# Performance work log

Measured on AMD Instinct MI355X. Metric: run time of the kernel, lower is better.

The kernel has to match this reference:

```python
import jax, jax.numpy as jnp
import numpy as np

B, T, D, V, LMAX = 16, 512, 256, 4233, 64
NEG = -1e30  # finite 'log zero' keeps grads NaN-free


def setup_inputs() -> dict:
    key = jax.random.key(0)
    k1, k2, k3, k4 = jax.random.split(key, 4)
    hs_pad = jax.random.normal(k1, (B, T, D), dtype=jnp.float32)
    hlens = jnp.full((B,), T, dtype=jnp.int32)
    ys_pad = jax.random.randint(k2, (B, LMAX), 1, V, dtype=jnp.int32)  # blank=0 excluded
    ys_lens = jax.random.randint(k3, (B,), LMAX // 2, LMAX + 1, dtype=jnp.int32)
    W = jax.random.normal(k4, (V, D), dtype=jnp.float32) * (1.0 / np.sqrt(D))
    b = jnp.zeros((V,), dtype=jnp.float32)
    return {"hs_pad": hs_pad, "hlens": hlens, "ys_pad": ys_pad,
            "ys_lens": ys_lens, "W": W, "b": b}


def _ctc_loss_sum(logp_tbv, ext, allow, hlens, ys_lens):
    """logp_tbv: [T,B,V] log-softmax; ext: [B,S] extended labels (blank-interleaved).
    Returns sum over batch of -log p(y|x) (torch CTCLoss reduction='sum')."""
    Tn, Bn, _ = logp_tbv.shape
    S = ext.shape[1]
    # per-frame log-prob of each extended label: [T,B,S]
    lp_ext = jnp.take_along_axis(
        logp_tbv, jnp.broadcast_to(ext[None], (Tn, Bn, S)), axis=2)

    # t = 0 init: alpha[0]=lp(blank), alpha[1]=lp(y_1)
    alpha0 = jnp.full((Bn, S), NEG, dtype=logp_tbv.dtype)
    alpha0 = alpha0.at[:, 0].set(lp_ext[0, :, 0])
    alpha0 = alpha0.at[:, 1].set(lp_ext[0, :, 1])

    def step(alpha, inp):
        lp_t, t = inp  # lp_t: [B,S]
        a1 = jnp.pad(alpha[:, :-1], ((0, 0), (1, 0)), constant_values=NEG)
        a2 = jnp.pad(alpha[:, :-2], ((0, 0), (2, 0)), constant_values=NEG)
        a2 = jnp.where(allow, a2, NEG)
        new = jnp.logaddexp(jnp.logaddexp(alpha, a1), a2) + lp_t
        alpha = jnp.where((t < hlens)[:, None], new, alpha)  # freeze past hlen
        return alpha, None

    ts = jnp.arange(1, Tn, dtype=jnp.int32)
    alpha, _ = jax.lax.scan(step, alpha0, (lp_ext[1:], ts))

    last = 2 * ys_lens  # index of final blank state
    bi = jnp.arange(Bn)
    ll = jnp.logaddexp(alpha[bi, last], alpha[bi, last - 1])
    return -jnp.sum(ll)


def reference(hs_pad, hlens, ys_pad, ys_lens, W, b):
    # linear projection + log_softmax (dropout_rate=0.0 -> identity)
    logits = jnp.einsum('btd,vd->btv', hs_pad, W) + b
    logp = jax.nn.log_softmax(logits, axis=-1)          # [B,T,V]
    logp = jnp.transpose(logp, (1, 0, 2))               # [T,B,V]

    Bn, Lmax = ys_pad.shape
    S = 2 * Lmax + 1
    ext = jnp.zeros((Bn, S), dtype=ys_pad.dtype).at[:, 1::2].set(ys_pad)
    prev2 = jnp.pad(ext, ((0, 0), (2, 0)))[:, :-2]
    allow = (ext != 0) & (ext != prev2) & (jnp.arange(S) >= 2)

    loss = _ctc_loss_sum(logp, ext, allow, hlens, ys_lens)
    return loss / Bn  # module divides by ys_hat.size(1) == batch
```

## Files before the change

kernel.cpp:

```cpp
#include <hip/hip_runtime.h>

constexpr int Bn = 16;
constexpr int Tn = 512;
constexpr int Dn = 256;
constexpr int Vn = 4233;
constexpr int Vp = 4352;
constexpr int Ln = 64;
constexpr int Un = 80;
constexpr int CS = 68;
constexpr int NCB = 34;
constexpr int Mtot = Bn * Tn;

#define LN2     0.6931471805599453f
#define INV_LN2 1.4426950408889634f

typedef __attribute__((ext_vector_type(8))) short short8;
typedef __attribute__((ext_vector_type(4))) float f32x4;

__device__ __forceinline__ float lg2(float x) { return __builtin_amdgcn_logf(x); }
__device__ __forceinline__ float ex2(float x) { return __builtin_amdgcn_exp2f(x); }

__device__ __forceinline__ unsigned short cvt_bf16(float f) {
    unsigned int u = __float_as_uint(f);
    u = (u + 0x7fffu + ((u >> 16) & 1u)) >> 16;
    return (unsigned short)u;
}

__device__ __forceinline__ void gl_lds16(const void* g, void* l) {
    __builtin_amdgcn_global_load_lds(
        (const __attribute__((address_space(1))) void*)g,
        (__attribute__((address_space(3))) void*)l,
        16, 0, 0);
}

__device__ __forceinline__ float dpp_shr1_f(float v, float edge) {
    return __int_as_float(__builtin_amdgcn_update_dpp(
        __float_as_int(edge), __float_as_int(v), 0x138, 0xF, 0xF, false));
}
__device__ __forceinline__ int dpp_shr1_i(int v, int edge) {
    return __builtin_amdgcn_update_dpp(edge, v, 0x138, 0xF, 0xF, false);
}

__global__ __launch_bounds__(256) void conv(
    const float* __restrict__ hs, const float* __restrict__ W,
    const float* __restrict__ bias, const int* __restrict__ ys,
    unsigned short* __restrict__ hs_b, unsigned short* __restrict__ w_b,
    float* __restrict__ gbias, float* __restrict__ out)
{
    const int gid = blockIdx.x * 256 + threadIdx.x;
    const int stride = gridDim.x * 256;
    const float4* hs4 = (const float4*)hs;
    const float4* W4  = (const float4*)W;

    if (gid == 0) out[0] = 0.0f;

    for (int i = gid; i < (Bn * Tn * Dn) / 4; i += stride) {
        float4 v = hs4[i];
        ushort4 o = make_ushort4(cvt_bf16(v.x), cvt_bf16(v.y), cvt_bf16(v.z), cvt_bf16(v.w));
        *(ushort4*)(&hs_b[i * 4]) = o;
    }
    for (int i = gid; i < Vp * (Dn / 4); i += stride) {
        int row = i >> 6;
        float4 v = make_float4(0.f, 0.f, 0.f, 0.f);
        if (row < Vn) v = W4[i];
        ushort4 o = make_ushort4(cvt_bf16(v.x), cvt_bf16(v.y), cvt_bf16(v.z), cvt_bf16(v.w));
        *(ushort4*)(&w_b[i * 4]) = o;
    }
    for (int i = gid; i < Bn * 128; i += stride) {
        int b = i >> 7;
        int u = i & 127;
        int v = (u == 0) ? 0 : ((u <= Ln) ? ys[b * Ln + u - 1] : -1);
        gbias[i] = (v >= 0) ? bias[v] : 0.0f;
    }
}

__global__ __launch_bounds__(256) void gemm_se(
    const unsigned short* __restrict__ hs_b, const unsigned short* __restrict__ w_b,
    const int* __restrict__ ys, const float* __restrict__ bias,
    const float* __restrict__ gbias, float* __restrict__ sep,
    float* __restrict__ glg2)
{
    __shared__ __align__(16) short lsA[128 * 64];
    __shared__ __align__(16) short lsB[128 * 64];

    const int tid = threadIdx.x;
    const int lane = tid & 63;
    const int w = tid >> 6;
    const int lr = lane & 15;
    const int kq = lane >> 4;
    const int m0 = blockIdx.x * 128;
    const int mw = w * 32;
    const bool gather = (blockIdx.y == NCB);
    const int b = blockIdx.x >> 2;

    const int srow = lane >> 3;
    const int scg  = (lane & 7) ^ (srow & 7);
    const int scol = scg * 8;

    const unsigned short* bptr[4];
    #pragma unroll
    for (int j = 0; j < 4; ++j) {
        int c = w * 4 + j;
        int row = c * 8 + srow;
        int v;
        if (gather) {
            if (row == 0) v = 0;
            else if (row <= Ln) v = ys[b * Ln + row - 1];
            else v = Vn + 32;
        } else {
            v = blockIdx.y * 128 + row;
        }
        bptr[j] = w_b + (size_t)v * Dn + scol;
    }

    f32x4 acc[2][8];
    #pragma unroll
    for (int mf = 0; mf < 2; ++mf)
        #pragma unroll
        for (int nf = 0; nf < 8; ++nf)
            acc[mf][nf] = (f32x4){0.f, 0.f, 0.f, 0.f};

    for (int ks = 0; ks < 4; ++ks) {
        const int k0 = ks * 64;
        __syncthreads();
        #pragma unroll
        for (int j = 0; j < 4; ++j) {
            int c = w * 4 + j;
            int row = c * 8 + srow;
            gl_lds16(hs_b + (size_t)(m0 + row) * Dn + k0 + scol, (char*)lsA + c * 1024);
            gl_lds16(bptr[j] + k0,                               (char*)lsB + c * 1024);
        }
        __syncthreads();

        #pragma unroll
        for (int sub = 0; sub < 2; ++sub) {
            short8 af[2], bf[8];
            #pragma unroll
            for (int mf = 0; mf < 2; ++mf) {
                int row = mw + mf * 16 + lr;
                int cg = (sub * 4 + kq) ^ (row & 7);
                af[mf] = *(const short8*)(&lsA[row * 64 + cg * 8]);
            }
            #pragma unroll
            for (int nf = 0; nf < 8; ++nf) {
                int row = nf * 16 + lr;
                int cg = (sub * 4 + kq) ^ (row & 7);
                bf[nf] = *(const short8*)(&lsB[row * 64 + cg * 8]);
            }
            #pragma unroll
            for (int mf = 0; mf < 2; ++mf)
                #pragma unroll
                for (int nf = 0; nf < 8; ++nf)
                    acc[mf][nf] = __builtin_amdgcn_mfma_f32_16x16x32_bf16(
                        af[mf], bf[nf], acc[mf][nf], 0, 0, 0);
        }
    }

    if (!gather) {
        const int n0 = blockIdx.y * 128;
        float bcol[8]; bool valid[8];
        #pragma unroll
        for (int nf = 0; nf < 8; ++nf) {
            int col = n0 + nf * 16 + lr;
            valid[nf] = (col < Vn);
            bcol[nf] = valid[nf] ? bias[col] : 0.0f;
        }
        #pragma unroll
        for (int mf = 0; mf < 2; ++mf) {
            #pragma unroll
            for (int r = 0; r < 4; ++r) {
                float s = 0.0f;
                #pragma unroll
                for (int nf = 0; nf < 8; ++nf)
                    if (valid[nf]) s += __expf(acc[mf][nf][r] + bcol[nf]);
                #pragma unroll
                for (int off = 1; off < 16; off <<= 1) s += __shfl_xor(s, off, 64);
                if (lr == 0)
                    sep[(size_t)blockIdx.y * Mtot + m0 + mw + mf * 16 + kq * 4 + r] = s;
            }
        }
    } else {
        #pragma unroll
        for (int mf = 0; mf < 2; ++mf) {
            #pragma unroll
            for (int nf = 0; nf < 5; ++nf) {
                int u = nf * 16 + lr;
                float gv = gbias[b * 128 + u];
                #pragma unroll
                for (int r = 0; r < 4; ++r) {
                    int g = m0 + mw + mf * 16 + kq * 4 + r;
                    glg2[(size_t)g * Un + u] = (acc[mf][nf][r] + gv) * INV_LN2;
                }
            }
        }
    }
}

__global__ __launch_bounds__(256) void lse_norm(
    const float* __restrict__ sep, float* __restrict__ glg2)
{
    __shared__ float sl[64];
    const int tid = threadIdx.x;
    const int g0 = blockIdx.x * 64;

    if (tid < 64) {
        float s = 0.0f;
        #pragma unroll
        for (int c = 0; c < NCB; ++c) s += sep[(size_t)c * Mtot + g0 + tid];
        sl[tid] = lg2(s);
    }
    __syncthreads();

    #pragma unroll
    for (int j = 0; j < 4; ++j) {
        int i = tid + j * 256;
        int row = i >> 4, u4 = (i & 15) * 4;
        float* p = glg2 + (size_t)(g0 + row) * Un + u4;
        float4 v = *(const float4*)p;
        float sub = sl[row];
        v.x = ex2(v.x - sub); v.y = ex2(v.y - sub);
        v.z = ex2(v.z - sub); v.w = ex2(v.w - sub);
        *(float4*)p = v;
    }
    if (tid < 64) {
        float* p = glg2 + (size_t)(g0 + tid) * Un + 64;
        *p = ex2(*p - sl[tid]);
    }
}

__global__ __launch_bounds__(256) void ctc_fwd(
    const float* __restrict__ pmat, const int* __restrict__ ys,
    const int* __restrict__ hlens, const int* __restrict__ ylens,
    float* __restrict__ out)
{
    __shared__ float ls[2][64 * CS + 4];
    __shared__ float shO[64], shE[64], shZ[64];
    __shared__ int   shX[64];

    const int b = blockIdx.x;
    const int tid = threadIdx.x;
    const int l = tid & 63;

    const int hl = hlens[b];
    int yl  = ys[b * Ln + l];
    int ylm = (l >= 1) ? ys[b * Ln + l - 1] : -1;
    const float aF = ((l >= 1) && (yl != ylm)) ? 1.0f : 0.0f;

    const float* pm = pmat + (size_t)b * Tn * Un;

    #pragma unroll
    for (int j = 0; j < 4; ++j) {
        int i = tid + j * 256;
        int tt = i >> 4, u4 = (i & 15) * 4;
        *(float4*)(&ls[0][tt * CS + u4]) = *(const float4*)(pm + (size_t)(1 + tt) * Un + u4);
    }
    if (tid < 64) ls[0][tid * CS + 64] = pm[(size_t)(1 + tid) * Un + 64];
    __syncthreads();

    float o = (l == 0) ? pm[1] : 0.0f;
    float e = (l == 0) ? pm[0] : 0.0f;
    float z = 0.0f;
    int ex = 0;
    int dn = 0;

    float4 r4a = make_float4(0.f,0.f,0.f,0.f), r4b = r4a, r4c = r4a, r4d = r4a;
    float r1 = 0.0f;

    float qa0, qa1, qa2, qa3, ra0, ra1, ra2, ra3;
    float qb0, qb1, qb2, qb3, rb0, rb1, rb2, rb3;
    float qc0, qc1, qc2, qc3, rc0, rc1, rc2, rc3;

#define RENORM do { \
        float mm = fmaxf(fmaxf(o, e), z); \
        bool nz = (mm > 0.0f); \
        int dd = nz ? ((int)((__float_as_uint(mm) >> 23) & 255u) - 127) : 0; \
        o = ldexpf(o, -dd); e = ldexpf(e, -dd); z = ldexpf(z, -dd); \
        int exT = ex + dd; \
        int xm1 = dpp_shr1_i(exT, -(1 << 28)); \
        int et = nz ? exT : xm1; \
        ex = et; \
        int xet = dpp_shr1_i(et, -(1 << 28)); \
        dn = xet - ex; \
    } while (0)

#define STEPR(qv, rv) do { \
        float om1 = dpp_shr1_f(o, 0.0f); \
        float an  = ldexpf(om1, dn); \
        float nO = fmaf(aF, an, o + e) * (rv); \
        float nE = (e + an) * (qv); \
        float nZ = (z + o) * (qv); \
        o = nO; e = nE; z = nZ; \
    } while (0)

#define LDA(base) do { \
        qa0 = buf[(base) * CS];       ra0 = buf[(base) * CS + 1 + l]; \
        qa1 = buf[((base)+1) * CS];   ra1 = buf[((base)+1) * CS + 1 + l]; \
        qa2 = buf[((base)+2) * CS];   ra2 = buf[((base)+2) * CS + 1 + l]; \
        qa3 = buf[((base)+3) * CS];   ra3 = buf[((base)+3) * CS + 1 + l]; \
    } while (0)
#define LDB(base) do { \
        qb0 = buf[(base) * CS];       rb0 = buf[(base) * CS + 1 + l]; \
        qb1 = buf[((base)+1) * CS];   rb1 = buf[((base)+1) * CS + 1 + l]; \
        qb2 = buf[((base)+2) * CS];   rb2 = buf[((base)+2) * CS + 1 + l]; \
        qb3 = buf[((base)+3) * CS];   rb3 = buf[((base)+3) * CS + 1 + l]; \
    } while (0)
#define LDC(base) do { \
        qc0 = buf[(base) * CS];       rc0 = buf[(base) * CS + 1 + l]; \
        qc1 = buf[((base)+1) * CS];   rc1 = buf[((base)+1) * CS + 1 + l]; \
        qc2 = buf[((base)+2) * CS];   rc2 = buf[((base)+2) * CS + 1 + l]; \
        qc3 = buf[((base)+3) * CS];   rc3 = buf[((base)+3) * CS + 1 + l]; \
    } while (0)

#define W4A do { RENORM; STEPR(qa0,ra0); STEPR(qa1,ra1); STEPR(qa2,ra2); STEPR(qa3,ra3); } while (0)
#define W4B do { RENORM; STEPR(qb0,rb0); STEPR(qb1,rb1); STEPR(qb2,rb2); STEPR(qb3,rb3); } while (0)
#define W4C do { RENORM; STEPR(qc0,rc0); STEPR(qc1,rc1); STEPR(qc2,rc2); STEPR(qc3,rc3); } while (0)

#define STEPS(Joff, ACT) do { \
        RENORM; \
        float q = buf[(Joff) * CS]; \
        float r = buf[(Joff) * CS + 1 + l]; \
        float om1 = dpp_shr1_f(o, 0.0f); \
        float an  = ldexpf(om1, dn); \
        float nO = fmaf(aF, an, o + e) * r; \
        float nE = (e + an) * q; \
        float nZ = (z + o) * q; \
        bool act = (ACT); \
        o = act ? nO : o; e = act ? nE : e; z = act ? nZ : z; \
    } while (0)

    for (int c = 0; c < 8; ++c) {
        if (c < 7) {
            const int tb = 1 + (c + 1) * 64;
            { int i = tid;       int tt = i >> 4, u4 = (i & 15) * 4;
              r4a = (tb + tt < Tn) ? *(const float4*)(pm + (size_t)(tb + tt) * Un + u4) : make_float4(0.f,0.f,0.f,0.f); }
            { int i = tid + 256; int tt = i >> 4, u4 = (i & 15) * 4;
              r4b = (tb + tt < Tn) ? *(const float4*)(pm + (size_t)(tb + tt) * Un + u4) : make_float4(0.f,0.f,0.f,0.f); }
            { int i = tid + 512; int tt = i >> 4, u4 = (i & 15) * 4;
              r4c = (tb + tt < Tn) ? *(const float4*)(pm + (size_t)(tb + tt) * Un + u4) : make_float4(0.f,0.f,0.f,0.f); }
            { int i = tid + 768; int tt = i >> 4, u4 = (i & 15) * 4;
              r4d = (tb + tt < Tn) ? *(const float4*)(pm + (size_t)(tb + tt) * Un + u4) : make_float4(0.f,0.f,0.f,0.f); }
            if (tid < 64)
                r1 = (tb + tid < Tn) ? pm[(size_t)(tb + tid) * Un + 64] : 0.0f;
        }

        const float* buf = ls[c & 1];

        if (c < 7) {
            if (hl >= (c + 1) * 64 + 1) {
                LDA(0); LDB(4);
                LDC(8);  W4A;
                LDA(12); W4B;
                LDB(16); W4C;
                LDC(20); W4A;
                LDA(24); W4B;
                LDB(28); W4C;
                LDC(32); W4A;
                LDA(36); W4B;
                LDB(40); W4C;
                LDC(44); W4A;
                LDA(48); W4B;
                LDB(52); W4C;
                LDC(56); W4A;
                LDA(60); W4B;
                W4C;
                W4A;
            } else {
                #pragma unroll 1
                for (int j = 0; j < 64; ++j)
                    STEPS(j, (c * 64 + 1 + j) < hl);
            }
        } else {
            if (hl >= Tn) {
                LDA(0); LDB(4);
                LDC(8);  W4A;
                LDA(12); W4B;
                LDB(16); W4C;
                LDC(20); W4A;
                LDA(24); W4B;
                LDB(28); W4C;
                LDC(32); W4A;
                LDA(36); W4B;
                LDB(40); W4C;
                LDC(44); W4A;
                LDA(48); W4B;
                LDB(52); W4C;
                LDC(56); W4A;
                LDA(60); W4B;
                W4C;
                RENORM;
                STEPR(qa0, ra0); STEPR(qa1, ra1); STEPR(qa2, ra2);
            } else {
                #pragma unroll 1
                for (int j = 0; j < 63; ++j)
                    STEPS(j, (449 + j) < hl);
            }
        }

        if (c < 7) {
            float* dst = ls[(c + 1) & 1];
            { int i = tid;       int tt = i >> 4, u4 = (i & 15) * 4; *(float4*)(&dst[tt * CS + u4]) = r4a; }
            { int i = tid + 256; int tt = i >> 4, u4 = (i & 15) * 4; *(float4*)(&dst[tt * CS + u4]) = r4b; }
            { int i = tid + 512; int tt = i >> 4, u4 = (i & 15) * 4; *(float4*)(&dst[tt * CS + u4]) = r4c; }
            { int i = tid + 768; int tt = i >> 4, u4 = (i & 15) * 4; *(float4*)(&dst[tt * CS + u4]) = r4d; }
            if (tid < 64) dst[tid * CS + 64] = r1;
        }
        __syncthreads();
    }
#undef RENORM
#undef STEPR
#undef LDA
#undef LDB
#undef LDC
#undef W4A
#undef W4B
#undef W4C
#undef STEPS

    if (tid < 64) { shO[l] = o; shE[l] = e; shZ[l] = z; shX[l] = ex; }
    __syncthreads();

    if (tid == 0) {
        int L = ylens[b];
        float vo = shO[L - 1]; int xo = shX[L - 1];
        float ve; int xe;
        if (L == 64) { ve = shZ[63]; xe = shX[63]; }
        else         { ve = shE[L];  xe = shX[L]; }
        int em = (xo > xe) ? xo : xe;
        float s = ldexpf(vo, xo - em) + ldexpf(ve, xe - em);
        float ll = (lg2(s) + (float)em) * LN2;
        atomicAdd(out, -ll / (float)Bn);
    }
}

extern "C" void kernel_launch(void* const* d_in, const int* in_sizes, int n_in,
                              void* d_out, int out_size, void* d_ws, size_t ws_size,
                              hipStream_t stream) {
    const float* hs    = (const float*)d_in[0];
    const int*   hlens = (const int*)d_in[1];
    const int*   ys    = (const int*)d_in[2];
    const int*   ylens = (const int*)d_in[3];
    const float* W     = (const float*)d_in[4];
    const float* bias  = (const float*)d_in[5];
    float* out = (float*)d_out;

    char* ws = (char*)d_ws;
    unsigned short* hs_b = (unsigned short*)(ws);
    unsigned short* w_b  = (unsigned short*)(ws + 4194304);
    float* glg2  = (float*)(ws + 6422528);
    float* sep   = (float*)(ws + 9043968);
    float* gbias = (float*)(ws + 10158080);

    conv<<<1024, 256, 0, stream>>>(hs, W, bias, ys, hs_b, w_b, gbias, out);
    gemm_se<<<dim3(64, NCB + 1), 256, 0, stream>>>(hs_b, w_b, ys, bias, gbias, sep, glg2);
    lse_norm<<<Mtot / 64, 256, 0, stream>>>(sep, glg2);
    ctc_fwd<<<Bn, 256, 0, stream>>>(glg2, ys, hlens, ylens, out);
}
```

Before: 123.8 us.

## Fuse GEMM, normalization and CTC forward into one persistent kernel with counters

Merges the GEMM/sum-exp, log-sum-exp normalization and CTC forward kernels into a single launch. The first 16 blocks run the CTC recursion and spin-wait on per-row-tile atomic counters, so each 128-row chunk can be consumed as soon as its GEMM blocks finish. The normalization pass is dropped: raw log2 gathered values are exponentiated on load, and the per-frame log-normalizer is summed by a helper wave and subtracted from the final log-likelihood. This removes two launches and a full read/write pass over the gathered probabilities. It relies on the CTC blocks being scheduled alongside the GEMM blocks without deadlock, and one wave now fetches while another accumulates corrections.

```diff
diff --git a/kernel.cpp b/kernel.cpp
--- a/kernel.cpp
+++ b/kernel.cpp
@@ -45,7 +45,7 @@
     const float* __restrict__ hs, const float* __restrict__ W,
     const float* __restrict__ bias, const int* __restrict__ ys,
     unsigned short* __restrict__ hs_b, unsigned short* __restrict__ w_b,
-    float* __restrict__ gbias, float* __restrict__ out)
+    float* __restrict__ gbias, float* __restrict__ out, int* __restrict__ cnt)
 {
     const int gid = blockIdx.x * 256 + threadIdx.x;
     const int stride = gridDim.x * 256;
@@ -53,6 +53,7 @@
     const float4* W4  = (const float4*)W;
 
     if (gid == 0) out[0] = 0.0f;
+    if (gid < 64) cnt[gid] = 0;
 
     for (int i = gid; i < (Bn * Tn * Dn) / 4; i += stride) {
         float4 v = hs4[i];
@@ -74,197 +75,183 @@
     }
 }
 
-__global__ __launch_bounds__(256) void gemm_se(
+__global__ __launch_bounds__(256) void mega(
     const unsigned short* __restrict__ hs_b, const unsigned short* __restrict__ w_b,
     const int* __restrict__ ys, const float* __restrict__ bias,
     const float* __restrict__ gbias, float* __restrict__ sep,
-    float* __restrict__ glg2)
+    float* __restrict__ glg2, const int* __restrict__ hlens,
+    const int* __restrict__ ylens, float* __restrict__ out,
+    int* __restrict__ cnt)
 {
-    __shared__ __align__(16) short lsA[128 * 64];
-    __shared__ __align__(16) short lsB[128 * 64];
+    __shared__ __align__(16) union SMem {
+        struct { short A[128 * 64]; short Bt[128 * 64]; } g;
+        struct {
+            float ls[2][64 * CS + 4];
+            float shO[64], shE[64], shZ[64];
+            int   shX[64];
+            float corr0, corrS;
+        } c;
+    } sm;
 
     const int tid = threadIdx.x;
     const int lane = tid & 63;
     const int w = tid >> 6;
-    const int lr = lane & 15;
-    const int kq = lane >> 4;
-    const int m0 = blockIdx.x * 128;
-    const int mw = w * 32;
-    const bool gather = (blockIdx.y == NCB);
-    const int b = blockIdx.x >> 2;
-
-    const int srow = lane >> 3;
-    const int scg  = (lane & 7) ^ (srow & 7);
-    const int scol = scg * 8;
-
-    const unsigned short* bptr[4];
-    #pragma unroll
-    for (int j = 0; j < 4; ++j) {
-        int c = w * 4 + j;
-        int row = c * 8 + srow;
-        int v;
-        if (gather) {
-            if (row == 0) v = 0;
-            else if (row <= Ln) v = ys[b * Ln + row - 1];
-            else v = Vn + 32;
-        } else {
-            v = blockIdx.y * 128 + row;
-        }
-        bptr[j] = w_b + (size_t)v * Dn + scol;
-    }
-
-    f32x4 acc[2][8];
-    #pragma unroll
-    for (int mf = 0; mf < 2; ++mf)
-        #pragma unroll
-        for (int nf = 0; nf < 8; ++nf)
-            acc[mf][nf] = (f32x4){0.f, 0.f, 0.f, 0.f};
-
-    for (int ks = 0; ks < 4; ++ks) {
-        const int k0 = ks * 64;
-        __syncthreads();
+
+    if (blockIdx.x >= 16) {
+        const int gidb = blockIdx.x - 16;
+        const int bx = gidb / 35;
+        const int by = gidb - bx * 35;
+        const bool gather = (by == NCB);
+        const int m0 = bx * 128;
+        const int mw = w * 32;
+        const int b = bx >> 2;
+        const int lr = lane & 15;
+        const int kq = lane >> 4;
+
+        const int srow = lane >> 3;
+        const int scg  = (lane & 7) ^ (srow & 7);
+        const int scol = scg * 8;
+
+        const unsigned short* bptr[4];
         #pragma unroll
         for (int j = 0; j < 4; ++j) {
             int c = w * 4 + j;
             int row = c * 8 + srow;
-            gl_lds16(hs_b + (size_t)(m0 + row) * Dn + k0 + scol, (char*)lsA + c * 1024);
-            gl_lds16(bptr[j] + k0,                               (char*)lsB + c * 1024);
+            int v;
+            if (gather) {
+                if (row == 0) v = 0;
+                else if (row <= Ln) v = ys[b * Ln + row - 1];
+                else v = Vn + 32;
+            } else {
+                v = by * 128 + row;
+            }
+            bptr[j] = w_b + (size_t)v * Dn + scol;
         }
+
+        f32x4 acc[2][8];
+        #pragma unroll
+        for (int mf = 0; mf < 2; ++mf)
+            #pragma unroll
+            for (int nf = 0; nf < 8; ++nf)
+                acc[mf][nf] = (f32x4){0.f, 0.f, 0.f, 0.f};
+
+        for (int ks = 0; ks < 4; ++ks) {
+            const int k0 = ks * 64;
+            __syncthreads();
+            #pragma unroll
+            for (int j = 0; j < 4; ++j) {
+                int c = w * 4 + j;
+                int row = c * 8 + srow;
+                gl_lds16(hs_b + (size_t)(m0 + row) * Dn + k0 + scol, (char*)sm.g.A  + c * 1024);
+                gl_lds16(bptr[j] + k0,                               (char*)sm.g.Bt + c * 1024);
+            }
+            __syncthreads();
+
+            #pragma unroll
+            for (int sub = 0; sub < 2; ++sub) {
+                short8 af[2], bf[8];
+                #pragma unroll
+                for (int mf = 0; mf < 2; ++mf) {
+                    int row = mw + mf * 16 + lr;
+                    int cg = (sub * 4 + kq) ^ (row & 7);
+                    af[mf] = *(const short8*)(&sm.g.A[row * 64 + cg * 8]);
+                }
+                #pragma unroll
+                for (int nf = 0; nf < 8; ++nf) {
+                    int row = nf * 16 + lr;
+                    int cg = (sub * 4 + kq) ^ (row & 7);
+                    bf[nf] = *(const short8*)(&sm.g.Bt[row * 64 + cg * 8]);
+                }
+                #pragma unroll
+                for (int mf = 0; mf < 2; ++mf)
+                    #pragma unroll
+                    for (int nf = 0; nf < 8; ++nf)
+                        acc[mf][nf] = __builtin_amdgcn_mfma_f32_16x16x32_bf16(
+                            af[mf], bf[nf], acc[mf][nf], 0, 0, 0);
+            }
+        }
+
+        if (!gather) {
+            const int n0 = by * 128;
+            float bcol[8]; bool valid[8];
+            #pragma unroll
+            for (int nf = 0; nf < 8; ++nf) {
+                int col = n0 + nf * 16 + lr;
+                valid[nf] = (col < Vn);
+                bcol[nf] = valid[nf] ? bias[col] : 0.0f;
+            }
+            #pragma unroll
+            for (int mf = 0; mf < 2; ++mf) {
+                #pragma unroll
+                for (int r = 0; r < 4; ++r) {
+                    float s = 0.0f;
+                    #pragma unroll
+                    for (int nf = 0; nf < 8; ++nf)
+                        if (valid[nf]) s += __expf(acc[mf][nf][r] + bcol[nf]);
+                    #pragma unroll
+                    for (int off = 1; off < 16; off <<= 1) s += __shfl_xor(s, off, 64);
+                    if (lr == 0)
+                        sep[(size_t)by * Mtot + m0 + mw + mf * 16 + kq * 4 + r] = s;
+                }
+            }
+        } else {
+            #pragma unroll
+            for (int mf = 0; mf < 2; ++mf) {
+                #pragma unroll
+                for (int nf = 0; nf < 5; ++nf) {
+                    int u = nf * 16 + lr;
+                    float gv = gbias[b * 128 + u];
+                    #pragma unroll
+                    for (int r = 0; r < 4; ++r) {
+                        int gm = m0 + mw + mf * 16 + kq * 4 + r;
+                        glg2[(size_t)gm * Un + u] = (acc[mf][nf][r] + gv) * INV_LN2;
+                    }
+                }
+            }
+        }
+
         __syncthreads();
-
-        #pragma unroll
-        for (int sub = 0; sub < 2; ++sub) {
-            short8 af[2], bf[8];
-            #pragma unroll
-            for (int mf = 0; mf < 2; ++mf) {
-                int row = mw + mf * 16 + lr;
-                int cg = (sub * 4 + kq) ^ (row & 7);
-                af[mf] = *(const short8*)(&lsA[row * 64 + cg * 8]);
-            }
-            #pragma unroll
-            for (int nf = 0; nf < 8; ++nf) {
-                int row = nf * 16 + lr;
-                int cg = (sub * 4 + kq) ^ (row & 7);
-                bf[nf] = *(const short8*)(&lsB[row * 64 + cg * 8]);
-            }
-            #pragma unroll
-            for (int mf = 0; mf < 2; ++mf)
-                #pragma unroll
-                for (int nf = 0; nf < 8; ++nf)
-                    acc[mf][nf] = __builtin_amdgcn_mfma_f32_16x16x32_bf16(
-                        af[mf], bf[nf], acc[mf][nf], 0, 0, 0);
-        }
-    }
-
-    if (!gather) {
-        const int n0 = blockIdx.y * 128;
-        float bcol[8]; bool valid[8];
-        #pragma unroll
-        for (int nf = 0; nf < 8; ++nf) {
-            int col = n0 + nf * 16 + lr;
-            valid[nf] = (col < Vn);
-            bcol[nf] = valid[nf] ? bias[col] : 0.0f;
-        }
-        #pragma unroll
-        for (int mf = 0; mf < 2; ++mf) {
-            #pragma unroll
-            for (int r = 0; r < 4; ++r) {
-                float s = 0.0f;
-                #pragma unroll
-                for (int nf = 0; nf < 8; ++nf)
-                    if (valid[nf]) s += __expf(acc[mf][nf][r] + bcol[nf]);
-                #pragma unroll
-                for (int off = 1; off < 16; off <<= 1) s += __shfl_xor(s, off, 64);
-                if (lr == 0)
-                    sep[(size_t)blockIdx.y * Mtot + m0 + mw + mf * 16 + kq * 4 + r] = s;
-            }
-        }
-    } else {
-        #pragma unroll
-        for (int mf = 0; mf < 2; ++mf) {
-            #pragma unroll
-            for (int nf = 0; nf < 5; ++nf) {
-                int u = nf * 16 + lr;
-                float gv = gbias[b * 128 + u];
-                #pragma unroll
-                for (int r = 0; r < 4; ++r) {
-                    int g = m0 + mw + mf * 16 + kq * 4 + r;
-                    glg2[(size_t)g * Un + u] = (acc[mf][nf][r] + gv) * INV_LN2;
-                }
-            }
-        }
-    }
-}
-
-__global__ __launch_bounds__(256) void lse_norm(
-    const float* __restrict__ sep, float* __restrict__ glg2)
-{
-    __shared__ float sl[64];
-    const int tid = threadIdx.x;
-    const int g0 = blockIdx.x * 64;
-
-    if (tid < 64) {
-        float s = 0.0f;
-        #pragma unroll
-        for (int c = 0; c < NCB; ++c) s += sep[(size_t)c * Mtot + g0 + tid];
-        sl[tid] = lg2(s);
-    }
-    __syncthreads();
-
-    #pragma unroll
-    for (int j = 0; j < 4; ++j) {
-        int i = tid + j * 256;
-        int row = i >> 4, u4 = (i & 15) * 4;
-        float* p = glg2 + (size_t)(g0 + row) * Un + u4;
-        float4 v = *(const float4*)p;
-        float sub = sl[row];
-        v.x = ex2(v.x - sub); v.y = ex2(v.y - sub);
-        v.z = ex2(v.z - sub); v.w = ex2(v.w - sub);
-        *(float4*)p = v;
-    }
-    if (tid < 64) {
-        float* p = glg2 + (size_t)(g0 + tid) * Un + 64;
-        *p = ex2(*p - sl[tid]);
-    }
-}
-
-__global__ __launch_bounds__(256) void ctc_fwd(
-    const float* __restrict__ pmat, const int* __restrict__ ys,
-    const int* __restrict__ hlens, const int* __restrict__ ylens,
-    float* __restrict__ out)
-{
-    __shared__ float ls[2][64 * CS + 4];
-    __shared__ float shO[64], shE[64], shZ[64];
-    __shared__ int   shX[64];
+        if (tid == 0)
+            __hip_atomic_fetch_add(&cnt[bx], 1, __ATOMIC_RELEASE, __HIP_MEMORY_SCOPE_AGENT);
+        return;
+    }
 
     const int b = blockIdx.x;
-    const int tid = threadIdx.x;
-    const int l = tid & 63;
+    const int l = lane;
 
     const int hl = hlens[b];
     int yl  = ys[b * Ln + l];
     int ylm = (l >= 1) ? ys[b * Ln + l - 1] : -1;
     const float aF = ((l >= 1) && (yl != ylm)) ? 1.0f : 0.0f;
 
-    const float* pm = pmat + (size_t)b * Tn * Un;
+    const float* pm = glg2 + (size_t)b * Tn * Un;
+
+    while (__hip_atomic_load(&cnt[b * 4], __ATOMIC_ACQUIRE, __HIP_MEMORY_SCOPE_AGENT) < 35)
+        __builtin_amdgcn_s_sleep(8);
 
     #pragma unroll
     for (int j = 0; j < 4; ++j) {
         int i = tid + j * 256;
         int tt = i >> 4, u4 = (i & 15) * 4;
-        *(float4*)(&ls[0][tt * CS + u4]) = *(const float4*)(pm + (size_t)(1 + tt) * Un + u4);
-    }
-    if (tid < 64) ls[0][tid * CS + 64] = pm[(size_t)(1 + tid) * Un + 64];
+        float4 v = *(const float4*)(pm + (size_t)(1 + tt) * Un + u4);
+        v.x = ex2(v.x); v.y = ex2(v.y); v.z = ex2(v.z); v.w = ex2(v.w);
+        *(float4*)(&sm.c.ls[0][tt * CS + u4]) = v;
+    }
+    if (tid < 64) sm.c.ls[0][tid * CS + 64] = ex2(pm[(size_t)(1 + tid) * Un + 64]);
+    if (tid == 128) {
+        float s0 = 0.0f;
+        #pragma unroll
+        for (int cb = 0; cb < NCB; ++cb) s0 += sep[(size_t)cb * Mtot + b * Tn];
+        sm.c.corr0 = lg2(s0);
+    }
     __syncthreads();
 
-    float o = (l == 0) ? pm[1] : 0.0f;
-    float e = (l == 0) ? pm[0] : 0.0f;
+    float o = (l == 0) ? ex2(pm[1]) : 0.0f;
+    float e = (l == 0) ? ex2(pm[0]) : 0.0f;
     float z = 0.0f;
     int ex = 0;
     int dn = 0;
-
-    float4 r4a = make_float4(0.f,0.f,0.f,0.f), r4b = r4a, r4c = r4a, r4d = r4a;
-    float r1 = 0.0f;
+    float corr = 0.0f;
 
     float qa0, qa1, qa2, qa3, ra0, ra1, ra2, ra3;
     float qb0, qb1, qb2, qb3, rb0, rb1, rb2, rb3;
@@ -329,80 +316,97 @@
     } while (0)
 
     for (int c = 0; c < 8; ++c) {
-        if (c < 7) {
-            const int tb = 1 + (c + 1) * 64;
-            { int i = tid;       int tt = i >> 4, u4 = (i & 15) * 4;
-              r4a = (tb + tt < Tn) ? *(const float4*)(pm + (size_t)(tb + tt) * Un + u4) : make_float4(0.f,0.f,0.f,0.f); }
-            { int i = tid + 256; int tt = i >> 4, u4 = (i & 15) * 4;
-              r4b = (tb + tt < Tn) ? *(const float4*)(pm + (size_t)(tb + tt) * Un + u4) : make_float4(0.f,0.f,0.f,0.f); }
-            { int i = tid + 512; int tt = i >> 4, u4 = (i & 15) * 4;
-              r4c = (tb + tt < Tn) ? *(const float4*)(pm + (size_t)(tb + tt) * Un + u4) : make_float4(0.f,0.f,0.f,0.f); }
-            { int i = tid + 768; int tt = i >> 4, u4 = (i & 15) * 4;
-              r4d = (tb + tt < Tn) ? *(const float4*)(pm + (size_t)(tb + tt) * Un + u4) : make_float4(0.f,0.f,0.f,0.f); }
-            if (tid < 64)
-                r1 = (tb + tid < Tn) ? pm[(size_t)(tb + tid) * Un + 64] : 0.0f;
-        }
-
-        const float* buf = ls[c & 1];
-
-        if (c < 7) {
-            if (hl >= (c + 1) * 64 + 1) {
-                LDA(0); LDB(4);
-                LDC(8);  W4A;
-                LDA(12); W4B;
-                LDB(16); W4C;
-                LDC(20); W4A;
-                LDA(24); W4B;
-                LDB(28); W4C;
-                LDC(32); W4A;
-                LDA(36); W4B;
-                LDB(40); W4C;
-                LDC(44); W4A;
-                LDA(48); W4B;
-                LDB(52); W4C;
-                LDC(56); W4A;
-                LDA(60); W4B;
-                W4C;
-                W4A;
+        if (w == 0) {
+            const float* buf = sm.c.ls[c & 1];
+            if (c < 7) {
+                if (hl >= (c + 1) * 64 + 1) {
+                    LDA(0); LDB(4);
+                    LDC(8);  W4A;
+                    LDA(12); W4B;
+                    LDB(16); W4C;
+                    LDC(20); W4A;
+                    LDA(24); W4B;
+                    LDB(28); W4C;
+                    LDC(32); W4A;
+                    LDA(36); W4B;
+                    LDB(40); W4C;
+                    LDC(44); W4A;
+                    LDA(48); W4B;
+                    LDB(52); W4C;
+                    LDC(56); W4A;
+                    LDA(60); W4B;
+                    W4C;
+                    W4A;
+                } else {
+                    #pragma unroll 1
+                    for (int j = 0; j < 64; ++j)
+                        STEPS(j, (c * 64 + 1 + j) < hl);
+                }
             } else {
-                #pragma unroll 1
-                for (int j = 0; j < 64; ++j)
-                    STEPS(j, (c * 64 + 1 + j) < hl);
+                if (hl >= Tn) {
+                    LDA(0); LDB(4);
+                    LDC(8);  W4A;
+                    LDA(12); W4B;
+                    LDB(16); W4C;
+                    LDC(20); W4A;
+                    LDA(24); W4B;
+                    LDB(28); W4C;
+                    LDC(32); W4A;
+                    LDA(36); W4B;
+                    LDB(40); W4C;
+                    LDC(44); W4A;
+                    LDA(48); W4B;
+                    LDB(52); W4C;
+                    LDC(56); W4A;
+                    LDA(60); W4B;
+                    W4C;
+                    RENORM;
+                    STEPR(qa0, ra0); STEPR(qa1, ra1); STEPR(qa2, ra2);
+                } else {
+                    #pragma unroll 1
+                    for (int j = 0; j < 63; ++j)
+                        STEPS(j, (449 + j) < hl);
+                }
             }
         } else {
-            if (hl >= Tn) {
-                LDA(0); LDB(4);
-                LDC(8);  W4A;
-                LDA(12); W4B;
-                LDB(16); W4C;
-                LDC(20); W4A;
-                LDA(24); W4B;
-                LDB(28); W4C;
-                LDC(32); W4A;
-                LDA(36); W4B;
-                LDB(40); W4C;
-                LDC(44); W4A;
-                LDA(48); W4B;
-                LDB(52); W4C;
-                LDC(56); W4A;
-                LDA(60); W4B;
-                W4C;
-                RENORM;
-                STEPR(qa0, ra0); STEPR(qa1, ra1); STEPR(qa2, ra2);
-            } else {
-                #pragma unroll 1
-                for (int j = 0; j < 63; ++j)
-                    STEPS(j, (449 + j) < hl);
-            }
-        }
-
-        if (c < 7) {
-            float* dst = ls[(c + 1) & 1];
-            { int i = tid;       int tt = i >> 4, u4 = (i & 15) * 4; *(float4*)(&dst[tt * CS + u4]) = r4a; }
-            { int i = tid + 256; int tt = i >> 4, u4 = (i & 15) * 4; *(float4*)(&dst[tt * CS + u4]) = r4b; }
-            { int i = tid + 512; int tt = i >> 4, u4 = (i & 15) * 4; *(float4*)(&dst[tt * CS + u4]) = r4c; }
-            { int i = tid + 768; int tt = i >> 4, u4 = (i & 15) * 4; *(float4*)(&dst[tt * CS + u4]) = r4d; }
-            if (tid < 64) dst[tid * CS + 64] = r1;
+            if (c < 7) {
+                int p = (c + 2) >> 1; if (p > 3) p = 3;
+                while (__hip_atomic_load(&cnt[b * 4 + p], __ATOMIC_ACQUIRE, __HIP_MEMORY_SCOPE_AGENT) < 35)
+                    __builtin_amdgcn_s_sleep(8);
+
+                const int tb = 1 + (c + 1) * 64;
+                float* dst = sm.c.ls[(c + 1) & 1];
+                const int t192 = tid - 64;
+                #pragma unroll
+                for (int j = 0; j < 6; ++j) {
+                    int i = t192 + j * 192;
+                    if (i < 1024) {
+                        int tt = i >> 4, u4 = (i & 15) * 4;
+                        float4 v;
+                        if (tb + tt < Tn) {
+                            v = *(const float4*)(pm + (size_t)(tb + tt) * Un + u4);
+                            v.x = ex2(v.x); v.y = ex2(v.y); v.z = ex2(v.z); v.w = ex2(v.w);
+                        } else {
+                            v = make_float4(0.f, 0.f, 0.f, 0.f);
+                        }
+                        *(float4*)(&dst[tt * CS + u4]) = v;
+                    }
+                }
+                if (t192 >= 128) {
+                    int tt = t192 - 128;
+                    dst[tt * CS + 64] = (tb + tt < Tn) ? ex2(pm[(size_t)(tb + tt) * Un + 64]) : 0.0f;
+                }
+            }
+            if (w == 1) {
+                int t = c * 64 + 1 + l;
+                if (t < hl) {
+                    float s = 0.0f;
+                    #pragma unroll
+                    for (int cb = 0; cb < NCB; ++cb)
+                        s += sep[(size_t)cb * Mtot + b * Tn + t];
+                    corr += lg2(s);
+                }
+            }
         }
         __syncthreads();
     }
@@ -416,18 +420,24 @@
 #undef W4C
 #undef STEPS
 
-    if (tid < 64) { shO[l] = o; shE[l] = e; shZ[l] = z; shX[l] = ex; }
+    if (tid < 64) { sm.c.shO[l] = o; sm.c.shE[l] = e; sm.c.shZ[l] = z; sm.c.shX[l] = ex; }
+    if (w == 1) {
+        #pragma unroll
+        for (int off = 1; off < 64; off <<= 1) corr += __shfl_xor(corr, off, 64);
+        if (l == 0) sm.c.corrS = corr;
+    }
     __syncthreads();
 
     if (tid == 0) {
         int L = ylens[b];
-        float vo = shO[L - 1]; int xo = shX[L - 1];
+        float vo = sm.c.shO[L - 1]; int xo = sm.c.shX[L - 1];
         float ve; int xe;
-        if (L == 64) { ve = shZ[63]; xe = shX[63]; }
-        else         { ve = shE[L];  xe = shX[L]; }
+        if (L == 64) { ve = sm.c.shZ[63]; xe = sm.c.shX[63]; }
+        else         { ve = sm.c.shE[L];  xe = sm.c.shX[L]; }
         int em = (xo > xe) ? xo : xe;
         float s = ldexpf(vo, xo - em) + ldexpf(ve, xe - em);
-        float ll = (lg2(s) + (float)em) * LN2;
+        float corrT = sm.c.corrS + sm.c.corr0;
+        float ll = (lg2(s) + (float)em - corrT) * LN2;
         atomicAdd(out, -ll / (float)Bn);
     }
 }
@@ -449,9 +459,9 @@
     float* glg2  = (float*)(ws + 6422528);
     float* sep   = (float*)(ws + 9043968);
     float* gbias = (float*)(ws + 10158080);
-
-    conv<<<1024, 256, 0, stream>>>(hs, W, bias, ys, hs_b, w_b, gbias, out);
-    gemm_se<<<dim3(64, NCB + 1), 256, 0, stream>>>(hs_b, w_b, ys, bias, gbias, sep, glg2);
-    lse_norm<<<Mtot / 64, 256, 0, stream>>>(sep, glg2);
-    ctc_fwd<<<Bn, 256, 0, stream>>>(glg2, ys, hlens, ylens, out);
-}
+    int*   cnt   = (int*)(ws + 10166272);
+
+    conv<<<1024, 256, 0, stream>>>(hs, W, bias, ys, hs_b, w_b, gbias, out, cnt);
+    mega<<<16 + 64 * (NCB + 1), 256, 0, stream>>>(
+        hs_b, w_b, ys, bias, gbias, sep, glg2, hlens, ylens, out, cnt);
+}
```

After: 167.3 us. +35.1%, slower.

## Run CTC alpha recursion in fp64 with wave-uniform renormalization every 32 steps

Applied to the files above, without the earlier changes.

Switches the CTC forward recursion state from fp32 with per-lane exponents, renormalised every 4 steps, to fp64 with one wave-wide exponent. Renormalisation now runs only every 32 steps and uses a DPP/readlane max reduction. The wider dynamic range of double lets the code drop the per-step ldexp shift between neighbouring lanes and most of the renorm overhead. The cost is fp64 arithmetic, two DPP moves per shift and higher register pressure, and fp64 throughput on the target may or may not offset the removed work.

```diff
diff --git a/kernel.cpp b/kernel.cpp
--- a/kernel.cpp
+++ b/kernel.cpp
@@ -33,12 +33,27 @@
         16, 0, 0);
 }
 
-__device__ __forceinline__ float dpp_shr1_f(float v, float edge) {
-    return __int_as_float(__builtin_amdgcn_update_dpp(
-        __float_as_int(edge), __float_as_int(v), 0x138, 0xF, 0xF, false));
-}
-__device__ __forceinline__ int dpp_shr1_i(int v, int edge) {
-    return __builtin_amdgcn_update_dpp(edge, v, 0x138, 0xF, 0xF, false);
+__device__ __forceinline__ double dpp_shr1_d(double v) {
+    union { double d; int i[2]; } u, r;
+    u.d = v;
+    r.i[0] = __builtin_amdgcn_update_dpp(0, u.i[0], 0x138, 0xF, 0xF, false);
+    r.i[1] = __builtin_amdgcn_update_dpp(0, u.i[1], 0x138, 0xF, 0xF, false);
+    return r.d;
+}
+
+__device__ __forceinline__ int wave_imax(int v) {
+    int t;
+    t = __builtin_amdgcn_update_dpp(v, v, 0xB1,  0xF, 0xF, false); v = (t > v) ? t : v;
+    t = __builtin_amdgcn_update_dpp(v, v, 0x4E,  0xF, 0xF, false); v = (t > v) ? t : v;
+    t = __builtin_amdgcn_update_dpp(v, v, 0x141, 0xF, 0xF, false); v = (t > v) ? t : v;
+    t = __builtin_amdgcn_update_dpp(v, v, 0x140, 0xF, 0xF, false); v = (t > v) ? t : v;
+    int a = __builtin_amdgcn_readlane(v, 0);
+    int b = __builtin_amdgcn_readlane(v, 16);
+    int c = __builtin_amdgcn_readlane(v, 32);
+    int d = __builtin_amdgcn_readlane(v, 48);
+    int ab = (a > b) ? a : b;
+    int cd = (c > d) ? c : d;
+    return (ab > cd) ? ab : cd;
 }
 
 __global__ __launch_bounds__(256) void conv(
@@ -234,7 +249,7 @@
     float* __restrict__ out)
 {
     __shared__ float ls[2][64 * CS + 4];
-    __shared__ float shO[64], shE[64], shZ[64];
+    __shared__ double shO[64], shE[64], shZ[64];
     __shared__ int   shX[64];
 
     const int b = blockIdx.x;
@@ -244,7 +259,7 @@
     const int hl = hlens[b];
     int yl  = ys[b * Ln + l];
     int ylm = (l >= 1) ? ys[b * Ln + l - 1] : -1;
-    const float aF = ((l >= 1) && (yl != ylm)) ? 1.0f : 0.0f;
+    const double aF = ((l >= 1) && (yl != ylm)) ? 1.0 : 0.0;
 
     const float* pm = pmat + (size_t)b * Tn * Un;
 
@@ -257,73 +272,66 @@
     if (tid < 64) ls[0][tid * CS + 64] = pm[(size_t)(1 + tid) * Un + 64];
     __syncthreads();
 
-    float o = (l == 0) ? pm[1] : 0.0f;
-    float e = (l == 0) ? pm[0] : 0.0f;
-    float z = 0.0f;
+    double o = (l == 0) ? (double)pm[1] : 0.0;
+    double e = (l == 0) ? (double)pm[0] : 0.0;
+    double z = 0.0;
     int ex = 0;
-    int dn = 0;
 
     float4 r4a = make_float4(0.f,0.f,0.f,0.f), r4b = r4a, r4c = r4a, r4d = r4a;
     float r1 = 0.0f;
 
-    float qa0, qa1, qa2, qa3, ra0, ra1, ra2, ra3;
-    float qb0, qb1, qb2, qb3, rb0, rb1, rb2, rb3;
-    float qc0, qc1, qc2, qc3, rc0, rc1, rc2, rc3;
-
-#define RENORM do { \
-        float mm = fmaxf(fmaxf(o, e), z); \
-        bool nz = (mm > 0.0f); \
-        int dd = nz ? ((int)((__float_as_uint(mm) >> 23) & 255u) - 127) : 0; \
-        o = ldexpf(o, -dd); e = ldexpf(e, -dd); z = ldexpf(z, -dd); \
-        int exT = ex + dd; \
-        int xm1 = dpp_shr1_i(exT, -(1 << 28)); \
-        int et = nz ? exT : xm1; \
-        ex = et; \
-        int xet = dpp_shr1_i(et, -(1 << 28)); \
-        dn = xet - ex; \
+    double qa0, qa1, qa2, qa3, ra0, ra1, ra2, ra3;
+    double qb0, qb1, qb2, qb3, rb0, rb1, rb2, rb3;
+    double qc0, qc1, qc2, qc3, rc0, rc1, rc2, rc3;
+
+#define RENORM32 do { \
+        double mm = fmax(fmax(o, e), z); \
+        union { double d; unsigned int ui[2]; } um; um.d = mm; \
+        int kk = (int)((um.ui[1] >> 20) & 2047u) - 1023; \
+        int km = wave_imax(kk); \
+        o = ldexp(o, -km); e = ldexp(e, -km); z = ldexp(z, -km); \
+        ex += km; \
     } while (0)
 
 #define STEPR(qv, rv) do { \
-        float om1 = dpp_shr1_f(o, 0.0f); \
-        float an  = ldexpf(om1, dn); \
-        float nO = fmaf(aF, an, o + e) * (rv); \
-        float nE = (e + an) * (qv); \
-        float nZ = (z + o) * (qv); \
+        double an = dpp_shr1_d(o); \
+        double nO = fma(aF, an, o + e) * (rv); \
+        double nE = (e + an) * (qv); \
+        double nZ = (z + o) * (qv); \
         o = nO; e = nE; z = nZ; \
     } while (0)
 
 #define LDA(base) do { \
-        qa0 = buf[(base) * CS];       ra0 = buf[(base) * CS + 1 + l]; \
-        qa1 = buf[((base)+1) * CS];   ra1 = buf[((base)+1) * CS + 1 + l]; \
-        qa2 = buf[((base)+2) * CS];   ra2 = buf[((base)+2) * CS + 1 + l]; \
-        qa3 = buf[((base)+3) * CS];   ra3 = buf[((base)+3) * CS + 1 + l]; \
+        qa0 = (double)buf[(base) * CS];       ra0 = (double)buf[(base) * CS + 1 + l]; \
+        qa1 = (double)buf[((base)+1) * CS];   ra1 = (double)buf[((base)+1) * CS + 1 + l]; \
+        qa2 = (double)buf[((base)+2) * CS];   ra2 = (double)buf[((base)+2) * CS + 1 + l]; \
+        qa3 = (double)buf[((base)+3) * CS];   ra3 = (double)buf[((base)+3) * CS + 1 + l]; \
     } while (0)
 #define LDB(base) do { \
-        qb0 = buf[(base) * CS];       rb0 = buf[(base) * CS + 1 + l]; \
-        qb1 = buf[((base)+1) * CS];   rb1 = buf[((base)+1) * CS + 1 + l]; \
-        qb2 = buf[((base)+2) * CS];   rb2 = buf[((base)+2) * CS + 1 + l]; \
-        qb3 = buf[((base)+3) * CS];   rb3 = buf[((base)+3) * CS + 1 + l]; \
+        qb0 = (double)buf[(base) * CS];       rb0 = (double)buf[(base) * CS + 1 + l]; \
+        qb1 = (double)buf[((base)+1) * CS];   rb1 = (double)buf[((base)+1) * CS + 1 + l]; \
+        qb2 = (double)buf[((base)+2) * CS];   rb2 = (double)buf[((base)+2) * CS + 1 + l]; \
+        qb3 = (double)buf[((base)+3) * CS];   rb3 = (double)buf[((base)+3) * CS + 1 + l]; \
     } while (0)
 #define LDC(base) do { \
-        qc0 = buf[(base) * CS];       rc0 = buf[(base) * CS + 1 + l]; \
-        qc1 = buf[((base)+1) * CS];   rc1 = buf[((base)+1) * CS + 1 + l]; \
-        qc2 = buf[((base)+2) * CS];   rc2 = buf[((base)+2) * CS + 1 + l]; \
-        qc3 = buf[((base)+3) * CS];   rc3 = buf[((base)+3) * CS + 1 + l]; \
-    } while (0)
-
-#define W4A do { RENORM; STEPR(qa0,ra0); STEPR(qa1,ra1); STEPR(qa2,ra2); STEPR(qa3,ra3); } while (0)
-#define W4B do { RENORM; STEPR(qb0,rb0); STEPR(qb1,rb1); STEPR(qb2,rb2); STEPR(qb3,rb3); } while (0)
-#define W4C do { RENORM; STEPR(qc0,rc0); STEPR(qc1,rc1); STEPR(qc2,rc2); STEPR(qc3,rc3); } while (0)
+        qc0 = (double)buf[(base) * CS];       rc0 = (double)buf[(base) * CS + 1 + l]; \
+        qc1 = (double)buf[((base)+1) * CS];   rc1 = (double)buf[((base)+1) * CS + 1 + l]; \
+        qc2 = (double)buf[((base)+2) * CS];   rc2 = (double)buf[((base)+2) * CS + 1 + l]; \
+        qc3 = (double)buf[((base)+3) * CS];   rc3 = (double)buf[((base)+3) * CS + 1 + l]; \
+    } while (0)
+
+#define W4A do { STEPR(qa0,ra0); STEPR(qa1,ra1); STEPR(qa2,ra2); STEPR(qa3,ra3); } while (0)
+#define W4B do { STEPR(qb0,rb0); STEPR(qb1,rb1); STEPR(qb2,rb2); STEPR(qb3,rb3); } while (0)
+#define W4C do { STEPR(qc0,rc0); STEPR(qc1,rc1); STEPR(qc2,rc2); STEPR(qc3,rc3); } while (0)
 
 #define STEPS(Joff, ACT) do { \
-        RENORM; \
-        float q = buf[(Joff) * CS]; \
-        float r = buf[(Joff) * CS + 1 + l]; \
-        float om1 = dpp_shr1_f(o, 0.0f); \
-        float an  = ldexpf(om1, dn); \
-        float nO = fmaf(aF, an, o + e) * r; \
-        float nE = (e + an) * q; \
-        float nZ = (z + o) * q; \
+        RENORM32; \
+        double q = (double)buf[(Joff) * CS]; \
+        double r = (double)buf[(Joff) * CS + 1 + l]; \
+        double an = dpp_shr1_d(o); \
+        double nO = fma(aF, an, o + e) * r; \
+        double nE = (e + an) * q; \
+        double nZ = (z + o) * q; \
         bool act = (ACT); \
         o = act ? nO : o; e = act ? nE : e; z = act ? nZ : z; \
     } while (0)
@@ -347,6 +355,7 @@
 
         if (c < 7) {
             if (hl >= (c + 1) * 64 + 1) {
+                RENORM32;
                 LDA(0); LDB(4);
                 LDC(8);  W4A;
                 LDA(12); W4B;
@@ -356,6 +365,7 @@
                 LDB(28); W4C;
                 LDC(32); W4A;
                 LDA(36); W4B;
+                RENORM32;
                 LDB(40); W4C;
                 LDC(44); W4A;
                 LDA(48); W4B;
@@ -371,6 +381,7 @@
             }
         } else {
             if (hl >= Tn) {
+                RENORM32;
                 LDA(0); LDB(4);
                 LDC(8);  W4A;
                 LDA(12); W4B;
@@ -380,6 +391,7 @@
                 LDB(28); W4C;
                 LDC(32); W4A;
                 LDA(36); W4B;
+                RENORM32;
                 LDB(40); W4C;
                 LDC(44); W4A;
                 LDA(48); W4B;
@@ -387,7 +399,6 @@
                 LDC(56); W4A;
                 LDA(60); W4B;
                 W4C;
-                RENORM;
                 STEPR(qa0, ra0); STEPR(qa1, ra1); STEPR(qa2, ra2);
             } else {
                 #pragma unroll 1
@@ -406,7 +417,7 @@
         }
         __syncthreads();
     }
-#undef RENORM
+#undef RENORM32
 #undef STEPR
 #undef LDA
 #undef LDB
@@ -421,13 +432,16 @@
 
     if (tid == 0) {
         int L = ylens[b];
-        float vo = shO[L - 1]; int xo = shX[L - 1];
-        float ve; int xe;
+        double vo = shO[L - 1]; int xo = shX[L - 1];
+        double ve; int xe;
         if (L == 64) { ve = shZ[63]; xe = shX[63]; }
         else         { ve = shE[L];  xe = shX[L]; }
         int em = (xo > xe) ? xo : xe;
-        float s = ldexpf(vo, xo - em) + ldexpf(ve, xe - em);
-        float ll = (lg2(s) + (float)em) * LN2;
+        double s = ldexp(vo, xo - em) + ldexp(ve, xe - em);
+        union { double d; unsigned int ui[2]; } us; us.d = s;
+        int ks = (int)((us.ui[1] >> 20) & 2047u) - 1023;
+        double mant = ldexp(s, -ks);
+        float ll = (lg2((float)mant) + (float)(ks + em)) * LN2;
         atomicAdd(out, -ll / (float)Bn);
     }
 }
```

After: 121.1 us. -2.2%, faster.
